# Optimization experiments

Hardware: AMD Instinct MI355X
Metric: run time of the kernel (lower is better)

Reference implementation:

```python
import jax, jax.numpy as jnp
import numpy as np

B, S, D, H = 2, 2048, 1024, 16
HD = D // H  # head dim = 64


def setup_inputs() -> dict:
    key = jax.random.key(0)
    ks = jax.random.split(key, 11)
    s = 0.02
    return {
        "query": jax.random.normal(ks[0], (B, S, D), jnp.float32),
        "key": jax.random.normal(ks[1], (B, S, D), jnp.float32),
        "value": jax.random.normal(ks[2], (B, S, D), jnp.float32),
        "Wq": jax.random.normal(ks[3], (D, D), jnp.float32) * s,
        "bq": jnp.zeros((D,), jnp.float32),
        "Wk": jax.random.normal(ks[4], (D, D), jnp.float32) * s,
        "bk": jnp.zeros((D,), jnp.float32),
        "Wv": jax.random.normal(ks[5], (D, D), jnp.float32) * s,
        "bv": jnp.zeros((D,), jnp.float32),
        "Wo": jax.random.normal(ks[6], (D, D), jnp.float32) * s,
        "bo": jnp.zeros((D,), jnp.float32),
    }


def reference(query, key, value, Wq, bq, Wk, bk, Wv, bv, Wo, bo):
    # Linear projections (torch Linear: x @ W^T + b; here W stored as [in, out])
    q = query @ Wq + bq  # [B,S,D]
    k = key @ Wk + bk
    v = value @ Wv + bv
    # split heads -> [B,H,S,HD]
    q = q.reshape(B, S, H, HD).transpose(0, 2, 1, 3)
    k = k.reshape(B, S, H, HD).transpose(0, 2, 1, 3)
    v = v.reshape(B, S, H, HD).transpose(0, 2, 1, 3)
    scores = jnp.einsum("bhqd,bhkd->bhqk", q, k) / jnp.sqrt(jnp.float32(HD))
    probs = jax.nn.softmax(scores, axis=-1)
    # dropout is identity at inference
    ctx = jnp.einsum("bhqk,bhkd->bhqd", probs, v)
    ctx = ctx.transpose(0, 2, 1, 3).reshape(B, S, D)
    return ctx @ Wo + bo
```

## Files before the change

### kernel.cpp

```cpp
#include <hip/hip_runtime.h>
#include <hip/hip_bf16.h>

#define BB 2
#define SS 2048
#define DD 1024
#define HH 16
#define HD 64
#define MM (BB*SS)

typedef __attribute__((ext_vector_type(8))) short bf16x8;
typedef __attribute__((ext_vector_type(4))) float f32x4;

static __device__ inline unsigned short f2bf(float x) {
    unsigned int u = __float_as_uint(x);
    unsigned int r = (u + 0x7fffu + ((u >> 16) & 1u)) >> 16;
    return (unsigned short)r;
}

static __device__ inline unsigned pack2bf(float lo, float hi) {
    union { __hip_bfloat162 h; unsigned u; } c;
    c.h = __float22bfloat162_rn(make_float2(lo, hi));
    return c.u;
}

static __device__ inline f32x4 mfma16(bf16x8 a, bf16x8 b, f32x4 c) {
    return __builtin_amdgcn_mfma_f32_16x16x32_bf16(a, b, c, 0, 0, 0);
}

static __device__ inline float fast_exp2(float x) {
    return __builtin_amdgcn_exp2f(x);
}

typedef __attribute__((address_space(3))) unsigned int lds_u32;
typedef const __attribute__((address_space(1))) unsigned int glb_u32;
static __device__ inline void async_ld16(const void* g, void* l) {
    __builtin_amdgcn_global_load_lds((glb_u32*)g, (lds_u32*)l, 16, 0, 0);
}

struct PrepArgs {
    const float* wsrc[4];
    unsigned short* wdst[4];
};
__global__ __launch_bounds__(256) void prep_inputs(PrepArgs args) {
    __shared__ float tile[32][33];
    const int z = blockIdx.z;
    const int t = threadIdx.x;
    const float* in = args.wsrc[z];
    unsigned short* out = args.wdst[z];
    const int c0 = blockIdx.x * 32, r0 = blockIdx.y * 32;
    {
        const int xf = (t & 7) * 4, yf = t >> 3;
        float4 v = *(const float4*)(in + (size_t)(r0 + yf) * DD + c0 + xf);
        tile[yf][xf + 0] = v.x;
        tile[yf][xf + 1] = v.y;
        tile[yf][xf + 2] = v.z;
        tile[yf][xf + 3] = v.w;
    }
    __syncthreads();
    {
        const int x8 = t & 7, y8 = t >> 3;
        uint2 w;
        w.x = pack2bf(tile[x8 * 4 + 0][y8], tile[x8 * 4 + 1][y8]);
        w.y = pack2bf(tile[x8 * 4 + 2][y8], tile[x8 * 4 + 3][y8]);
        *(uint2*)(out + (size_t)(c0 + y8) * DD + r0 + x8 * 4) = w;
    }
}

struct QKVArgs {
    const float* Af[3];
    const unsigned short* Bt[3];
    const float* bias[3];
    unsigned short* C[3];
};

#define QSCALE 0.1803368801111204f

#define NKT 16

__global__ __launch_bounds__(512, 2) void gemm_qkv(QKVArgs args) {
    __shared__ alignas(16) unsigned short AS[2][256 * 64];
    __shared__ alignas(16) unsigned short BS[2][256 * 64];
    const int lin = blockIdx.x;
    const int swz = (lin & 7) * 24 + (lin >> 3);
    const int z  = swz >> 6;
    const int by = (swz >> 2) & 15;
    const int bx = swz & 3;
    const float scale = (z == 0) ? QSCALE : 1.0f;
    const float* __restrict__ Af = args.Af[z];
    const unsigned short* __restrict__ Bt = args.Bt[z];
    const float* __restrict__ bias = args.bias[z];
    unsigned short* __restrict__ C = args.C[z];
    const int K = DD, N = DD;
    const int t = threadIdx.x;
    const int lane = t & 63, wave = t >> 6;
    const int quad = lane >> 4, l15 = lane & 15;
    const int wm = wave & 1, wn = wave >> 1;
    const int m0 = by * 256, n0 = bx * 256;

    const int srow = t >> 3;
    const int cslot = (t & 7) ^ (srow & 7);
    const unsigned short* gB = Bt + (size_t)(n0 + srow) * K + cslot * 8;
    const int dstoff = srow * 64 + (t & 7) * 8;

    auto stageB = [&](int tl, int h) {
        unsigned short* d = &BS[tl & 1][h * 128 * 64 + dstoff];
        const unsigned short* s = gB + (size_t)(h * 128) * K + (size_t)tl * 64;
        async_ld16(s, d);
        async_ld16(s + (size_t)64 * K, d + 64 * 64);
    };

    const int ar_ = t >> 3, as_ = t & 7;
    const int sw = as_ ^ (ar_ & 7);
    const float* gA0 = Af + (size_t)(m0 + 0 * 64 + ar_) * K + sw * 8;
    const float* gA1 = Af + (size_t)(m0 + 1 * 64 + ar_) * K + sw * 8;
    const float* gA2 = Af + (size_t)(m0 + 2 * 64 + ar_) * K + sw * 8;
    const float* gA3 = Af + (size_t)(m0 + 3 * 64 + ar_) * K + sw * 8;

    float4 fA0[8], fA1[8];
#define ISSUE_A(buf_, tl_)                                                    \
    {                                                                         \
        const size_t ko_ = (size_t)(tl_) * 64;                                \
        buf_[0] = *(const float4*)(gA0 + ko_);                                \
        buf_[1] = *(const float4*)(gA0 + ko_ + 4);                            \
        buf_[2] = *(const float4*)(gA1 + ko_);                                \
        buf_[3] = *(const float4*)(gA1 + ko_ + 4);                            \
        buf_[4] = *(const float4*)(gA2 + ko_);                                \
        buf_[5] = *(const float4*)(gA2 + ko_ + 4);                            \
        buf_[6] = *(const float4*)(gA3 + ko_);                                \
        buf_[7] = *(const float4*)(gA3 + ko_ + 4);                            \
    }
#define CVT_WRITE_A(buf_, tl_)                                                \
    {                                                                         \
        _Pragma("unroll")                                                     \
        for (int h = 0; h < 4; h++) {                                         \
            uint4 w_;                                                         \
            w_.x = pack2bf(buf_[h * 2].x, buf_[h * 2].y);                     \
            w_.y = pack2bf(buf_[h * 2].z, buf_[h * 2].w);                     \
            w_.z = pack2bf(buf_[h * 2 + 1].x, buf_[h * 2 + 1].y);             \
            w_.w = pack2bf(buf_[h * 2 + 1].z, buf_[h * 2 + 1].w);             \
            *(uint4*)&AS[(tl_) & 1][(h * 64 + ar_) * 64 + as_ * 8] = w_;      \
        }                                                                     \
    }

    ISSUE_A(fA0, 0);
    stageB(0, 0); stageB(0, 1);
    ISSUE_A(fA1, 1);
    asm volatile("s_waitcnt vmcnt(8)" ::: "memory");
    CVT_WRITE_A(fA0, 0);
    asm volatile("s_waitcnt lgkmcnt(0)" ::: "memory");
    __builtin_amdgcn_s_barrier();

    f32x4 acc[8][4];
#pragma unroll
    for (int i = 0; i < 8; i++)
#pragma unroll
        for (int j = 0; j < 4; j++) acc[i][j] = (f32x4){0.f, 0.f, 0.f, 0.f};

#pragma unroll 2
    for (int kt = 0; kt < NKT; ++kt) {
        if (kt > 0) {
            if (kt < NKT - 1) asm volatile("s_waitcnt vmcnt(8) lgkmcnt(0)" ::: "memory");
            else              asm volatile("s_waitcnt vmcnt(0) lgkmcnt(0)" ::: "memory");
            __builtin_amdgcn_s_barrier();
        }

        const unsigned short* Ab = AS[kt & 1];
        const unsigned short* Bb = BS[kt & 1];
        bf16x8 af[4][2], bf[4][2];

#pragma unroll
        for (int i = 0; i < 4; i++) {
            const int row = wm * 128 + i * 16 + l15;
#pragma unroll
            for (int kk = 0; kk < 2; kk++)
                af[i][kk] = *(const bf16x8*)&Ab[row * 64 + ((kk * 4 + quad) ^ (l15 & 7)) * 8];
        }
#pragma unroll
        for (int j = 0; j < 2; j++) {
            const int row = wn * 64 + j * 16 + l15;
#pragma unroll
            for (int kk = 0; kk < 2; kk++)
                bf[j][kk] = *(const bf16x8*)&Bb[row * 64 + ((kk * 4 + quad) ^ (l15 & 7)) * 8];
        }
        if (kt + 1 < NKT) { stageB(kt + 1, 0); stageB(kt + 1, 1); }
        __builtin_amdgcn_s_barrier();
        __builtin_amdgcn_s_setprio(1);
#pragma unroll
        for (int i = 0; i < 4; i++)
#pragma unroll
            for (int j = 0; j < 2; j++) {
                acc[i][j] = mfma16(af[i][0], bf[j][0], acc[i][j]);
                acc[i][j] = mfma16(af[i][1], bf[j][1], acc[i][j]);
            }
        __builtin_amdgcn_s_setprio(0);
        __builtin_amdgcn_s_barrier();

#pragma unroll
        for (int j = 2; j < 4; j++) {
            const int row = wn * 64 + j * 16 + l15;
#pragma unroll
            for (int kk = 0; kk < 2; kk++)
                bf[j][kk] = *(const bf16x8*)&Bb[row * 64 + ((kk * 4 + quad) ^ (l15 & 7)) * 8];
        }
        __builtin_amdgcn_s_barrier();
        __builtin_amdgcn_s_setprio(1);
#pragma unroll
        for (int i = 0; i < 4; i++)
#pragma unroll
            for (int j = 2; j < 4; j++) {
                acc[i][j] = mfma16(af[i][0], bf[j][0], acc[i][j]);
                acc[i][j] = mfma16(af[i][1], bf[j][1], acc[i][j]);
            }
        __builtin_amdgcn_s_setprio(0);
        __builtin_amdgcn_s_barrier();

#pragma unroll
        for (int i = 0; i < 4; i++) {
            const int row = wm * 128 + 64 + i * 16 + l15;
#pragma unroll
            for (int kk = 0; kk < 2; kk++)
                af[i][kk] = *(const bf16x8*)&Ab[row * 64 + ((kk * 4 + quad) ^ (l15 & 7)) * 8];
        }
        __builtin_amdgcn_s_barrier();
        __builtin_amdgcn_s_setprio(1);
#pragma unroll
        for (int i = 0; i < 4; i++)
#pragma unroll
            for (int j = 0; j < 2; j++) {
                acc[4 + i][j] = mfma16(af[i][0], bf[j][0], acc[4 + i][j]);
                acc[4 + i][j] = mfma16(af[i][1], bf[j][1], acc[4 + i][j]);
            }
        __builtin_amdgcn_s_setprio(0);
        __builtin_amdgcn_s_barrier();

        if (kt + 1 < NKT) {
            CVT_WRITE_A(fA1, kt + 1);
            if (kt + 2 < NKT) ISSUE_A(fA1, kt + 2);
        }
        __builtin_amdgcn_s_barrier();
        __builtin_amdgcn_s_setprio(1);
#pragma unroll
        for (int i = 0; i < 4; i++)
#pragma unroll
            for (int j = 2; j < 4; j++) {
                acc[4 + i][j] = mfma16(af[i][0], bf[j][0], acc[4 + i][j]);
                acc[4 + i][j] = mfma16(af[i][1], bf[j][1], acc[4 + i][j]);
            }
        __builtin_amdgcn_s_setprio(0);
    }

    if (z == 2) {
#pragma unroll
        for (int j = 0; j < 4; j++) {
            int col = n0 + wn * 64 + j * 16 + l15;
            float bv = bias[col];
#pragma unroll
            for (int i = 0; i < 8; i++) {
                int rowb = m0 + wm * 128 + i * 16 + quad * 4;
                int b = rowb >> 11, s = rowb & (SS - 1);
                uint2 w;
                w.x = pack2bf(acc[i][j][0] + bv, acc[i][j][1] + bv);
                w.y = pack2bf(acc[i][j][2] + bv, acc[i][j][3] + bv);
                *(uint2*)(C + (size_t)b * DD * SS + (size_t)col * SS + s) = w;
            }
        }
    } else {
#pragma unroll
        for (int j = 0; j < 4; j++) {
            int col = n0 + wn * 64 + j * 16 + l15;
            float bv = bias[col];
#pragma unroll
            for (int i = 0; i < 8; i++) {
                int rowb = m0 + wm * 128 + i * 16 + quad * 4;
#pragma unroll
                for (int rr = 0; rr < 4; rr++) {
                    float v = (acc[i][j][rr] + bv) * scale;
                    C[(size_t)(rowb + rr) * N + col] = f2bf(v);
                }
            }
        }
    }
#undef ISSUE_A
#undef CVT_WRITE_A
}

#define ONKT 16

__global__ __launch_bounds__(256, 2) void gemm_out(const unsigned short* __restrict__ A,
                                                   const unsigned short* __restrict__ Bt,
                                                   const float* __restrict__ bias,
                                                   float* __restrict__ C) {
    __shared__ alignas(16) unsigned short AS[2][128 * 64];
    __shared__ alignas(16) unsigned short BS[2][128 * 64];
    const int t = threadIdx.x;
    const int lane = t & 63, wave = t >> 6;
    const int quad = lane >> 4, l15 = lane & 15;
    const int wm = wave & 1, wn = wave >> 1;
    const int lin = blockIdx.x;
    const int swz = (lin & 7) * 32 + (lin >> 3);
    const int bx = swz & 7, by = swz >> 3;
    const int m0 = by * 128, n0 = bx * 128;
    const int K = DD, N = DD;

    const int srow = t >> 3;
    const int cslot = (t & 7) ^ (srow & 7);
    const unsigned short* gA = A + (size_t)(m0 + srow) * K + cslot * 8;
    const unsigned short* gB = Bt + (size_t)(n0 + srow) * K + cslot * 8;
    const int dstoff = srow * 64 + (t & 7) * 8;

    auto stageA = [&](int tl) {
        unsigned short* d = &AS[tl & 1][dstoff];
        const unsigned short* s = gA + (size_t)tl * 64;
#pragma unroll
        for (int r = 0; r < 4; r++)
            async_ld16(s + (size_t)(r * 32) * K, d + r * 32 * 64);
    };
    auto stageB = [&](int tl) {
        unsigned short* d = &BS[tl & 1][dstoff];
        const unsigned short* s = gB + (size_t)tl * 64;
#pragma unroll
        for (int r = 0; r < 4; r++)
            async_ld16(s + (size_t)(r * 32) * K, d + r * 32 * 64);
    };

    stageA(0); stageB(0); stageA(1);

    f32x4 acc[4][4];
#pragma unroll
    for (int i = 0; i < 4; i++)
#pragma unroll
        for (int j = 0; j < 4; j++) acc[i][j] = (f32x4){0.f, 0.f, 0.f, 0.f};

#pragma unroll 2
    for (int kt = 0; kt < ONKT; ++kt) {
        if (kt < ONKT - 1) asm volatile("s_waitcnt vmcnt(4)" ::: "memory");
        else               asm volatile("s_waitcnt vmcnt(0)" ::: "memory");
        __builtin_amdgcn_s_barrier();

        const unsigned short* Ab = AS[kt & 1];
        const unsigned short* Bb = BS[kt & 1];
        bf16x8 af[4][2], bf[4][2];

#pragma unroll
        for (int i = 0; i < 4; i++) {
            const int row = wm * 64 + i * 16 + l15;
#pragma unroll
            for (int kk = 0; kk < 2; kk++)
                af[i][kk] = *(const bf16x8*)&Ab[row * 64 + ((kk * 4 + quad) ^ (l15 & 7)) * 8];
        }
#pragma unroll
        for (int j = 0; j < 2; j++) {
            const int row = wn * 64 + j * 16 + l15;
#pragma unroll
            for (int kk = 0; kk < 2; kk++)
                bf[j][kk] = *(const bf16x8*)&Bb[row * 64 + ((kk * 4 + quad) ^ (l15 & 7)) * 8];
        }
        if (kt + 1 < ONKT) stageB(kt + 1);
        __builtin_amdgcn_s_barrier();
        __builtin_amdgcn_s_setprio(1);
#pragma unroll
        for (int i = 0; i < 4; i++)
#pragma unroll
            for (int j = 0; j < 2; j++) {
                acc[i][j] = mfma16(af[i][0], bf[j][0], acc[i][j]);
                acc[i][j] = mfma16(af[i][1], bf[j][1], acc[i][j]);
            }
        __builtin_amdgcn_s_setprio(0);
        __builtin_amdgcn_s_barrier();

#pragma unroll
        for (int j = 2; j < 4; j++) {
            const int row = wn * 64 + j * 16 + l15;
#pragma unroll
            for (int kk = 0; kk < 2; kk++)
                bf[j][kk] = *(const bf16x8*)&Bb[row * 64 + ((kk * 4 + quad) ^ (l15 & 7)) * 8];
        }
        if (kt + 2 < ONKT) stageA(kt + 2);
        __builtin_amdgcn_s_barrier();
        __builtin_amdgcn_s_setprio(1);
#pragma unroll
        for (int i = 0; i < 4; i++)
#pragma unroll
            for (int j = 2; j < 4; j++) {
                acc[i][j] = mfma16(af[i][0], bf[j][0], acc[i][j]);
                acc[i][j] = mfma16(af[i][1], bf[j][1], acc[i][j]);
            }
        __builtin_amdgcn_s_setprio(0);
    }

#pragma unroll
    for (int j = 0; j < 4; j++) {
        int col = n0 + wn * 64 + j * 16 + l15;
        float bv = bias[col];
#pragma unroll
        for (int i = 0; i < 4; i++) {
            int rowb = m0 + wm * 64 + i * 16 + quad * 4;
#pragma unroll
            for (int rr = 0; rr < 4; rr++)
                C[(size_t)(rowb + rr) * N + col] = acc[i][j][rr] + bv;
        }
    }
}

#define TK 64
#define NTILE (SS / TK)
#define LDP 72

__global__ __launch_bounds__(256, 2) void flash_attn(const unsigned short* __restrict__ Q,
                                                     const unsigned short* __restrict__ Kg,
                                                     const unsigned short* __restrict__ Vt,
                                                     unsigned short* __restrict__ ctx) {
    __shared__ alignas(16) unsigned short Ks[3][TK * LDP];
    __shared__ alignas(16) unsigned short Vs[3][TK * LDP];
    const int t = threadIdx.x;
    const int lane = t & 63, wave = t >> 6;
    const int quad = lane >> 4, l15 = lane & 15;
    const int swz = (blockIdx.x & 7) * 64 + (blockIdx.x >> 3);
    const int qg = swz & 15;
    const int bh = swz >> 4;
    const int h = bh & 15, b = bh >> 4;
    const int q0 = (qg * 4 + wave) * 32;

    const unsigned short* Qb = Q + (size_t)b * SS * DD + h * HD;
    const unsigned short* Kb = Kg + (size_t)b * SS * DD + h * HD;
    const unsigned short* Vb = Vt + ((size_t)b * DD + h * HD) * SS;

    const int r0 = t >> 3, cs = t & 7;
    const unsigned short* gK = Kb + (size_t)r0 * DD + cs * 8;
    const unsigned short* gV = Vb + (size_t)r0 * SS + cs * 8;
    const int ldsoff0 = r0 * LDP + cs * 8;
    const int ldsoff1 = (r0 + 32) * LDP + cs * 8;

    bf16x8 qa[2][2];
#pragma unroll
    for (int qt = 0; qt < 2; qt++) {
        qa[qt][0] = *(const bf16x8*)(Qb + (size_t)(q0 + qt * 16 + l15) * DD + quad * 8);
        qa[qt][1] = *(const bf16x8*)(Qb + (size_t)(q0 + qt * 16 + l15) * DD + 32 + quad * 8);
    }

    float lrow[2] = {0.f, 0.f};
    f32x4 o[2][4];
#pragma unroll
    for (int qt = 0; qt < 2; qt++)
#pragma unroll
        for (int j = 0; j < 4; j++) o[qt][j] = (f32x4){0.f, 0.f, 0.f, 0.f};

    {
        uint4 kr0 = *(const uint4*)(gK);
        uint4 kr1 = *(const uint4*)(gK + (size_t)32 * DD);
        uint4 vr0 = *(const uint4*)(gV);
        uint4 vr1 = *(const uint4*)(gV + (size_t)32 * SS);
        *(uint4*)&Ks[0][ldsoff0] = kr0;
        *(uint4*)&Ks[0][ldsoff1] = kr1;
        *(uint4*)&Vs[0][ldsoff0] = vr0;
        *(uint4*)&Vs[0][ldsoff1] = vr1;
    }
    __syncthreads();

    int rb = 0;
    for (int tile = 0; tile < NTILE; ++tile) {
        uint4 kr0, kr1, vr0, vr1;
        if (tile + 1 < NTILE) {
            const unsigned short* gKn = gK + (size_t)(tile + 1) * TK * DD;
            const unsigned short* gVn = gV + (tile + 1) * TK;
            kr0 = *(const uint4*)(gKn);
            kr1 = *(const uint4*)(gKn + (size_t)32 * DD);
            vr0 = *(const uint4*)(gVn);
            vr1 = *(const uint4*)(gVn + (size_t)32 * SS);
        }
        const unsigned short* Ksb = Ks[rb];
        const unsigned short* Vsb = Vs[rb];
#pragma unroll
        for (int half = 0; half < 2; half++) {
            const int kb0 = half * 32;
            bf16x8 k0 = *(const bf16x8*)&Ksb[(kb0 + l15) * LDP + quad * 8];
            bf16x8 k1 = *(const bf16x8*)&Ksb[(kb0 + l15) * LDP + 32 + quad * 8];
            bf16x8 k2 = *(const bf16x8*)&Ksb[(kb0 + 16 + l15) * LDP + quad * 8];
            bf16x8 k3 = *(const bf16x8*)&Ksb[(kb0 + 16 + l15) * LDP + 32 + quad * 8];
            union { ushort4 s[2]; bf16x8 v; } af[4];
#pragma unroll
            for (int j = 0; j < 4; j++) {
                af[j].s[0] = *(const ushort4*)&Vsb[(j * 16 + l15) * LDP + kb0 + quad * 4];
                af[j].s[1] = *(const ushort4*)&Vsb[(j * 16 + l15) * LDP + kb0 + 16 + quad * 4];
            }
#pragma unroll
            for (int qt = 0; qt < 2; qt++) {
                f32x4 sc0 = (f32x4){0.f, 0.f, 0.f, 0.f};
                f32x4 sc1 = (f32x4){0.f, 0.f, 0.f, 0.f};
                sc0 = mfma16(k0, qa[qt][0], sc0);
                sc0 = mfma16(k1, qa[qt][1], sc0);
                sc1 = mfma16(k2, qa[qt][0], sc1);
                sc1 = mfma16(k3, qa[qt][1], sc1);

                float p[8];
#pragma unroll
                for (int rr = 0; rr < 4; rr++) {
                    p[rr]     = fast_exp2(sc0[rr]);
                    p[rr + 4] = fast_exp2(sc1[rr]);
                }
                lrow[qt] += (p[0] + p[1]) + (p[2] + p[3]) + (p[4] + p[5]) + (p[6] + p[7]);

                union { unsigned u[4]; bf16x8 v; } pf;
                pf.u[0] = pack2bf(p[0], p[1]);
                pf.u[1] = pack2bf(p[2], p[3]);
                pf.u[2] = pack2bf(p[4], p[5]);
                pf.u[3] = pack2bf(p[6], p[7]);

#pragma unroll
                for (int j = 0; j < 4; j++)
                    o[qt][j] = mfma16(af[j].v, pf.v, o[qt][j]);
            }
        }
        if (tile + 1 < NTILE) {
            int wb = rb + 1; if (wb == 3) wb = 0;
            *(uint4*)&Ks[wb][ldsoff0] = kr0;
            *(uint4*)&Ks[wb][ldsoff1] = kr1;
            *(uint4*)&Vs[wb][ldsoff0] = vr0;
            *(uint4*)&Vs[wb][ldsoff1] = vr1;
            __syncthreads();
            rb = wb;
        }
    }

#pragma unroll
    for (int qt = 0; qt < 2; qt++) {
        float l = lrow[qt];
        l += __shfl_xor(l, 16, 64);
        l += __shfl_xor(l, 32, 64);
        float linv = 1.0f / l;
        unsigned short* crow = ctx + ((size_t)b * SS + q0 + qt * 16 + l15) * DD + h * HD;
#pragma unroll
        for (int j = 0; j < 4; j++) {
            uint2 w;
            w.x = pack2bf(o[qt][j][0] * linv, o[qt][j][1] * linv);
            w.y = pack2bf(o[qt][j][2] * linv, o[qt][j][3] * linv);
            *(uint2*)(crow + j * 16 + quad * 4) = w;
        }
    }
}

extern "C" void kernel_launch(void* const* d_in, const int* in_sizes, int n_in,
                              void* d_out, int out_size, void* d_ws, size_t ws_size,
                              hipStream_t stream) {
    const float* query = (const float*)d_in[0];
    const float* key   = (const float*)d_in[1];
    const float* value = (const float*)d_in[2];
    const float* Wq = (const float*)d_in[3];
    const float* bq = (const float*)d_in[4];
    const float* Wk = (const float*)d_in[5];
    const float* bk = (const float*)d_in[6];
    const float* Wv = (const float*)d_in[7];
    const float* bv = (const float*)d_in[8];
    const float* Wo = (const float*)d_in[9];
    const float* bo = (const float*)d_in[10];
    float* out = (float*)d_out;

    char* ws = (char*)d_ws;
    const size_t WSZ = (size_t)DD * DD * 2;
    const size_t XSZ = (size_t)MM * DD * 2;
    unsigned short* Wqt = (unsigned short*)(ws + 0 * WSZ);
    unsigned short* Wkt = (unsigned short*)(ws + 1 * WSZ);
    unsigned short* Wvt = (unsigned short*)(ws + 2 * WSZ);
    unsigned short* Wot = (unsigned short*)(ws + 3 * WSZ);
    unsigned short* Qp  = (unsigned short*)(ws + 4 * WSZ + 0 * XSZ);
    unsigned short* Kp  = (unsigned short*)(ws + 4 * WSZ + 1 * XSZ);
    unsigned short* Vtp = (unsigned short*)(ws + 4 * WSZ + 2 * XSZ);
    unsigned short* ctx = (unsigned short*)(ws + 4 * WSZ + 3 * XSZ);

    PrepArgs pargs;
    pargs.wsrc[0] = Wq; pargs.wsrc[1] = Wk; pargs.wsrc[2] = Wv; pargs.wsrc[3] = Wo;
    pargs.wdst[0] = Wqt; pargs.wdst[1] = Wkt; pargs.wdst[2] = Wvt; pargs.wdst[3] = Wot;
    prep_inputs<<<dim3(32, 32, 4), 256, 0, stream>>>(pargs);

    QKVArgs args;
    args.Af[0] = query; args.Af[1] = key; args.Af[2] = value;
    args.Bt[0] = Wqt; args.Bt[1] = Wkt; args.Bt[2] = Wvt;
    args.bias[0] = bq; args.bias[1] = bk; args.bias[2] = bv;
    args.C[0] = Qp; args.C[1] = Kp; args.C[2] = Vtp;
    gemm_qkv<<<(DD / 256) * (MM / 256) * 3, 512, 0, stream>>>(args);

    flash_attn<<<BB * HH * 16, 256, 0, stream>>>(Qp, Kp, Vtp, ctx);

    gemm_out<<<(DD / 128) * (MM / 128), 256, 0, stream>>>(ctx, Wot, bo, out);
}
```

Before: 227.5 us.

## Switch flash attention inner loop to 32x32x16 MFMA with lane-swap P repack

The attention kernel now computes scores and P·V with 32x32x16 bf16 MFMA instructions instead of 16x16x32, so each wave handles a 32-row query block as a single tile. The score accumulator layout is rearranged into the B-operand layout with cross-half lane shuffles instead of going through shared memory. The aim is fewer MFMA issues and fewer LDS fragment loads per tile, with s_setprio hints around the MFMA groups. In exchange it adds shuffle work per tile and raises register pressure from the 16-wide accumulators.

```diff
diff --git a/kernel.cpp b/kernel.cpp
--- a/kernel.cpp
+++ b/kernel.cpp
@@ -10,6 +10,7 @@
 
 typedef __attribute__((ext_vector_type(8))) short bf16x8;
 typedef __attribute__((ext_vector_type(4))) float f32x4;
+typedef __attribute__((ext_vector_type(16))) float f32x16;
 
 static __device__ inline unsigned short f2bf(float x) {
     unsigned int u = __float_as_uint(x);
@@ -26,6 +27,9 @@
 static __device__ inline f32x4 mfma16(bf16x8 a, bf16x8 b, f32x4 c) {
     return __builtin_amdgcn_mfma_f32_16x16x32_bf16(a, b, c, 0, 0, 0);
 }
+static __device__ inline f32x16 mfma32(bf16x8 a, bf16x8 b, f32x16 c) {
+    return __builtin_amdgcn_mfma_f32_32x32x16_bf16(a, b, c, 0, 0, 0);
+}
 
 static __device__ inline float fast_exp2(float x) {
     return __builtin_amdgcn_exp2f(x);
@@ -35,6 +39,15 @@
 typedef const __attribute__((address_space(1))) unsigned int glb_u32;
 static __device__ inline void async_ld16(const void* g, void* l) {
     __builtin_amdgcn_global_load_lds((glb_u32*)g, (lds_u32*)l, 16, 0, 0);
+}
+
+static __device__ inline void half_swap(unsigned& a, unsigned& b) {
+    const int hi = (int)(threadIdx.x & 32);
+    unsigned ax = (unsigned)__shfl_xor((int)a, 32, 64);
+    unsigned bx = (unsigned)__shfl_xor((int)b, 32, 64);
+    unsigned na = hi ? bx : a;
+    unsigned nb = hi ? b : ax;
+    a = na; b = nb;
 }
 
 struct PrepArgs {
@@ -414,7 +427,7 @@
     __shared__ alignas(16) unsigned short Vs[3][TK * LDP];
     const int t = threadIdx.x;
     const int lane = t & 63, wave = t >> 6;
-    const int quad = lane >> 4, l15 = lane & 15;
+    const int l31 = lane & 31, ch = lane >> 5;
     const int swz = (blockIdx.x & 7) * 64 + (blockIdx.x >> 3);
     const int qg = swz & 15;
     const int bh = swz >> 4;
@@ -431,19 +444,15 @@
     const int ldsoff0 = r0 * LDP + cs * 8;
     const int ldsoff1 = (r0 + 32) * LDP + cs * 8;
 
-    bf16x8 qa[2][2];
-#pragma unroll
-    for (int qt = 0; qt < 2; qt++) {
-        qa[qt][0] = *(const bf16x8*)(Qb + (size_t)(q0 + qt * 16 + l15) * DD + quad * 8);
-        qa[qt][1] = *(const bf16x8*)(Qb + (size_t)(q0 + qt * 16 + l15) * DD + 32 + quad * 8);
-    }
-
-    float lrow[2] = {0.f, 0.f};
-    f32x4 o[2][4];
-#pragma unroll
-    for (int qt = 0; qt < 2; qt++)
-#pragma unroll
-        for (int j = 0; j < 4; j++) o[qt][j] = (f32x4){0.f, 0.f, 0.f, 0.f};
+    bf16x8 qa[4];
+#pragma unroll
+    for (int d4 = 0; d4 < 4; d4++)
+        qa[d4] = *(const bf16x8*)(Qb + (size_t)(q0 + l31) * DD + d4 * 16 + ch * 8);
+
+    float lrow = 0.f;
+    f32x16 o0, o1;
+#pragma unroll
+    for (int i = 0; i < 16; i++) { o0[i] = 0.f; o1[i] = 0.f; }
 
     {
         uint4 kr0 = *(const uint4*)(gK);
@@ -470,47 +479,55 @@
         }
         const unsigned short* Ksb = Ks[rb];
         const unsigned short* Vsb = Vs[rb];
-#pragma unroll
-        for (int half = 0; half < 2; half++) {
-            const int kb0 = half * 32;
-            bf16x8 k0 = *(const bf16x8*)&Ksb[(kb0 + l15) * LDP + quad * 8];
-            bf16x8 k1 = *(const bf16x8*)&Ksb[(kb0 + l15) * LDP + 32 + quad * 8];
-            bf16x8 k2 = *(const bf16x8*)&Ksb[(kb0 + 16 + l15) * LDP + quad * 8];
-            bf16x8 k3 = *(const bf16x8*)&Ksb[(kb0 + 16 + l15) * LDP + 32 + quad * 8];
-            union { ushort4 s[2]; bf16x8 v; } af[4];
-#pragma unroll
-            for (int j = 0; j < 4; j++) {
-                af[j].s[0] = *(const ushort4*)&Vsb[(j * 16 + l15) * LDP + kb0 + quad * 4];
-                af[j].s[1] = *(const ushort4*)&Vsb[(j * 16 + l15) * LDP + kb0 + 16 + quad * 4];
-            }
-#pragma unroll
-            for (int qt = 0; qt < 2; qt++) {
-                f32x4 sc0 = (f32x4){0.f, 0.f, 0.f, 0.f};
-                f32x4 sc1 = (f32x4){0.f, 0.f, 0.f, 0.f};
-                sc0 = mfma16(k0, qa[qt][0], sc0);
-                sc0 = mfma16(k1, qa[qt][1], sc0);
-                sc1 = mfma16(k2, qa[qt][0], sc1);
-                sc1 = mfma16(k3, qa[qt][1], sc1);
-
-                float p[8];
-#pragma unroll
-                for (int rr = 0; rr < 4; rr++) {
-                    p[rr]     = fast_exp2(sc0[rr]);
-                    p[rr + 4] = fast_exp2(sc1[rr]);
-                }
-                lrow[qt] += (p[0] + p[1]) + (p[2] + p[3]) + (p[4] + p[5]) + (p[6] + p[7]);
-
-                union { unsigned u[4]; bf16x8 v; } pf;
-                pf.u[0] = pack2bf(p[0], p[1]);
-                pf.u[1] = pack2bf(p[2], p[3]);
-                pf.u[2] = pack2bf(p[4], p[5]);
-                pf.u[3] = pack2bf(p[6], p[7]);
-
-#pragma unroll
-                for (int j = 0; j < 4; j++)
-                    o[qt][j] = mfma16(af[j].v, pf.v, o[qt][j]);
-            }
-        }
+
+#pragma unroll
+        for (int st = 0; st < 2; st++) {
+            bf16x8 ka[4];
+#pragma unroll
+            for (int d4 = 0; d4 < 4; d4++)
+                ka[d4] = *(const bf16x8*)&Ksb[(st * 32 + l31) * LDP + d4 * 16 + ch * 8];
+            f32x16 sc;
+#pragma unroll
+            for (int i = 0; i < 16; i++) sc[i] = 0.f;
+            __builtin_amdgcn_s_setprio(1);
+            sc = mfma32(ka[0], qa[0], sc);
+            sc = mfma32(ka[1], qa[1], sc);
+            sc = mfma32(ka[2], qa[2], sc);
+            sc = mfma32(ka[3], qa[3], sc);
+            __builtin_amdgcn_s_setprio(0);
+
+            float p[16];
+#pragma unroll
+            for (int i = 0; i < 16; i++) p[i] = fast_exp2(sc[i]);
+            lrow += (((p[0] + p[1]) + (p[2] + p[3])) + ((p[4] + p[5]) + (p[6] + p[7])))
+                  + (((p[8] + p[9]) + (p[10] + p[11])) + ((p[12] + p[13]) + (p[14] + p[15])));
+
+            unsigned cA0 = pack2bf(p[0], p[1]),   cC0 = pack2bf(p[2], p[3]);
+            unsigned cB0 = pack2bf(p[4], p[5]),   cD0 = pack2bf(p[6], p[7]);
+            half_swap(cA0, cB0);
+            half_swap(cC0, cD0);
+            union { unsigned u[4]; bf16x8 v; } f0;
+            f0.u[0] = cA0; f0.u[1] = cC0; f0.u[2] = cB0; f0.u[3] = cD0;
+
+            unsigned cA1 = pack2bf(p[8], p[9]),   cC1 = pack2bf(p[10], p[11]);
+            unsigned cB1 = pack2bf(p[12], p[13]), cD1 = pack2bf(p[14], p[15]);
+            half_swap(cA1, cB1);
+            half_swap(cC1, cD1);
+            union { unsigned u[4]; bf16x8 v; } f1;
+            f1.u[0] = cA1; f1.u[1] = cC1; f1.u[2] = cB1; f1.u[3] = cD1;
+
+            bf16x8 v00 = *(const bf16x8*)&Vsb[(0 * 32 + l31) * LDP + st * 32 + ch * 8];
+            bf16x8 v01 = *(const bf16x8*)&Vsb[(0 * 32 + l31) * LDP + st * 32 + 16 + ch * 8];
+            bf16x8 v10 = *(const bf16x8*)&Vsb[(1 * 32 + l31) * LDP + st * 32 + ch * 8];
+            bf16x8 v11 = *(const bf16x8*)&Vsb[(1 * 32 + l31) * LDP + st * 32 + 16 + ch * 8];
+            __builtin_amdgcn_s_setprio(1);
+            o0 = mfma32(v00, f0.v, o0);
+            o0 = mfma32(v01, f1.v, o0);
+            o1 = mfma32(v10, f0.v, o1);
+            o1 = mfma32(v11, f1.v, o1);
+            __builtin_amdgcn_s_setprio(0);
+        }
+
         if (tile + 1 < NTILE) {
             int wb = rb + 1; if (wb == 3) wb = 0;
             *(uint4*)&Ks[wb][ldsoff0] = kr0;
@@ -522,19 +539,24 @@
         }
     }
 
-#pragma unroll
-    for (int qt = 0; qt < 2; qt++) {
-        float l = lrow[qt];
-        l += __shfl_xor(l, 16, 64);
-        l += __shfl_xor(l, 32, 64);
-        float linv = 1.0f / l;
-        unsigned short* crow = ctx + ((size_t)b * SS + q0 + qt * 16 + l15) * DD + h * HD;
-#pragma unroll
-        for (int j = 0; j < 4; j++) {
+    lrow += __shfl_xor(lrow, 32, 64);
+    const float linv = 1.0f / lrow;
+    unsigned short* crow = ctx + ((size_t)b * SS + q0 + l31) * DD + h * HD;
+#pragma unroll
+    for (int q4 = 0; q4 < 4; q4++) {
+        {
+            const int hd0 = 8 * q4 + 4 * ch;
             uint2 w;
-            w.x = pack2bf(o[qt][j][0] * linv, o[qt][j][1] * linv);
-            w.y = pack2bf(o[qt][j][2] * linv, o[qt][j][3] * linv);
-            *(uint2*)(crow + j * 16 + quad * 4) = w;
+            w.x = pack2bf(o0[q4 * 4 + 0] * linv, o0[q4 * 4 + 1] * linv);
+            w.y = pack2bf(o0[q4 * 4 + 2] * linv, o0[q4 * 4 + 3] * linv);
+            *(uint2*)(crow + hd0) = w;
+        }
+        {
+            const int hd0 = 8 * q4 + 4 * ch + 32;
+            uint2 w;
+            w.x = pack2bf(o1[q4 * 4 + 0] * linv, o1[q4 * 4 + 1] * linv);
+            w.y = pack2bf(o1[q4 * 4 + 2] * linv, o1[q4 * 4 + 3] * linv);
+            *(uint2*)(crow + hd0) = w;
         }
     }
 }
```

Measured after the change: 223.1 us. Within noise of the previous version (-1.9%).
